# Kernel optimization log

Hardware: AMD Instinct MI355X
Metric: run time of the kernel (lower is better)

The kernel has to match this reference:

```python
import jax, jax.numpy as jnp
import numpy as np

N = 10000      # nodes
E = 100000     # edges
C = 32         # in_channels == hidden_channels == out_channels
ED = 4         # edge_dim
G = 64         # number of graphs in the batch
EPS = 1e-5     # BatchNorm eps


def setup_inputs() -> dict:
    key = jax.random.key(0)
    ks = jax.random.split(key, 20)
    rn = lambda k, shape, s=0.05: jax.random.normal(k, shape, dtype=jnp.float32) * s
    return {
        "x": jax.random.normal(ks[0], (N, C), dtype=jnp.float32),
        "edge_attr": jax.random.normal(ks[1], (E, ED), dtype=jnp.float32),
        # edge MLP 1: ED -> C -> C*C ; NNConv1 root/bias
        "e1_w1": rn(ks[2], (ED, C)), "e1_b1": jnp.zeros((C,), jnp.float32),
        "e1_w2": rn(ks[3], (C, C * C)), "e1_b2": jnp.zeros((C * C,), jnp.float32),
        "root1": rn(ks[4], (C, C)), "bias1": jnp.zeros((C,), jnp.float32),
        # edge MLP 2: ED -> C -> C*C ; NNConv2 root/bias
        "e2_w1": rn(ks[5], (ED, C)), "e2_b1": jnp.zeros((C,), jnp.float32),
        "e2_w2": rn(ks[6], (C, C * C)), "e2_b2": jnp.zeros((C * C,), jnp.float32),
        "root2": rn(ks[7], (C, C)), "bias2": jnp.zeros((C,), jnp.float32),
        # BatchNorm (eval mode: running stats)
        "bn1_g": jnp.ones((C,), jnp.float32), "bn1_b": jnp.zeros((C,), jnp.float32),
        "bn1_m": rn(ks[8], (C,), 0.1), "bn1_v": 1.0 + 0.1 * jax.random.uniform(ks[9], (C,), dtype=jnp.float32),
        "bn2_g": jnp.ones((C,), jnp.float32), "bn2_b": jnp.zeros((C,), jnp.float32),
        "bn2_m": rn(ks[10], (C,), 0.1), "bn2_v": 1.0 + 0.1 * jax.random.uniform(ks[11], (C,), dtype=jnp.float32),
        # readout: C -> C//2 -> 1
        "r1_w": rn(ks[12], (C, C // 2)), "r1_b": jnp.zeros((C // 2,), jnp.float32),
        "r2_w": rn(ks[13], (C // 2, 1)), "r2_b": jnp.zeros((1,), jnp.float32),
        "edge_index": jax.random.randint(ks[14], (2, E), 0, N),
        "batch": jnp.sort(jax.random.randint(ks[15], (N,), 0, G)),
    }


def _nnconv(x, edge_index, edge_attr, w1, b1, w2, b2, root, bias):
    # edge MLP -> per-edge weight matrix [E, C, C]
    h = jax.nn.relu(edge_attr @ w1 + b1)
    W = (h @ w2 + b2).reshape(E, C, C)
    src, dst = edge_index[0], edge_index[1]
    # gather source features, per-edge matmul, scatter-mean to target nodes
    msg = jnp.einsum('ei,eio->eo', x[src], W)                      # [E, C]
    agg = jax.ops.segment_sum(msg, dst, num_segments=N)            # [N, C]
    cnt = jax.ops.segment_sum(jnp.ones((E,), x.dtype), dst, num_segments=N)
    agg = agg / jnp.maximum(cnt, 1.0)[:, None]
    return agg + x @ root + bias


def _bn(x, g, b, m, v):
    return (x - m) * jax.lax.rsqrt(v + EPS) * g + b


def reference(x, edge_attr,
              e1_w1, e1_b1, e1_w2, e1_b2, root1, bias1,
              e2_w1, e2_b1, e2_w2, e2_b2, root2, bias2,
              bn1_g, bn1_b, bn1_m, bn1_v,
              bn2_g, bn2_b, bn2_m, bn2_v,
              r1_w, r1_b, r2_w, r2_b,
              edge_index, batch):
    h = jax.nn.relu(_bn(_nnconv(x, edge_index, edge_attr, e1_w1, e1_b1, e1_w2, e1_b2, root1, bias1),
                        bn1_g, bn1_b, bn1_m, bn1_v))
    h = jax.nn.relu(_bn(_nnconv(h, edge_index, edge_attr, e2_w1, e2_b1, e2_w2, e2_b2, root2, bias2),
                        bn2_g, bn2_b, bn2_m, bn2_v))
    # global mean pool over graphs
    psum = jax.ops.segment_sum(h, batch, num_segments=G)           # [G, C]
    pcnt = jax.ops.segment_sum(jnp.ones((N,), h.dtype), batch, num_segments=G)
    pooled = psum / jnp.maximum(pcnt, 1.0)[:, None]
    # readout MLP (dropout is identity in eval)
    return jax.nn.relu(pooled @ r1_w + r1_b) @ r2_w + r2_b          # [G, 1]
```

## Files before the change

### kernel.cpp

```cpp
#include <hip/hip_runtime.h>

#define NN 10000
#define EE 100000
#define CC 32
#define GG 64
#define EPSV 1e-5f
#define NB 8
#define SLOTS 1056
#define HST 36
#define PST 36
#define PNODE (32*PST)

__global__ void k_hist(const int* __restrict__ ei,
                       int* __restrict__ cnt, int* __restrict__ deg) {
    int t = blockIdx.x * blockDim.x + threadIdx.x;
    if (t < EE) { atomicAdd(&cnt[ei[EE + t]], 1); atomicAdd(&deg[ei[t]], 1); }
}

__global__ __launch_bounds__(1024) void k_scan(const int* __restrict__ deg,
                                               int* __restrict__ rowptr) {
    __shared__ int buf[1024];
    int t = threadIdx.x;
    int v[10]; int s = 0;
    int base = t * 10;
    #pragma unroll
    for (int k = 0; k < 10; k++) {
        int idx = base + k;
        v[k] = (idx < NN) ? deg[idx] : 0;
        s += v[k];
    }
    buf[t] = s;
    for (int off = 1; off < 1024; off <<= 1) {
        __syncthreads();
        int val = buf[t] + ((t >= off) ? buf[t - off] : 0);
        __syncthreads();
        buf[t] = val;
    }
    __syncthreads();
    int carry = (t > 0) ? buf[t - 1] : 0;
    #pragma unroll
    for (int k = 0; k < 10; k++) {
        int idx = base + k;
        if (idx < NN) rowptr[idx] = carry;
        carry += v[k];
    }
    if (t == 1023) rowptr[NN] = buf[1023];
}

__global__ void k_scatter(const int* __restrict__ ei, const int* __restrict__ rowptr,
                          int* __restrict__ cursor, int* __restrict__ csr_eid) {
    int e = blockIdx.x * blockDim.x + threadIdx.x;
    if (e >= EE) return;
    int s = ei[e];
    int pos = atomicAdd(&cursor[s], 1);
    csr_eid[rowptr[s] + pos] = e;
}

__global__ void k_w2t(const float* __restrict__ w2a, const float* __restrict__ b2a,
                      const float* __restrict__ w2b, const float* __restrict__ b2b,
                      float* __restrict__ w2r1, float* __restrict__ w2r2) {
    int s = blockIdx.x * 256 + threadIdx.x;
    int i = blockIdx.y;
    if (s >= SLOTS) return;
    float va = (s < 1024) ? w2a[(s >> 5) * 1024 + i * 32 + (s & 31)]
                          : b2a[i * 32 + (s - 1024)];
    float vb = (s < 1024) ? w2b[(s >> 5) * 1024 + i * 32 + (s & 31)]
                          : b2b[i * 32 + (s - 1024)];
    w2r1[i * SLOTS + s] = va;
    w2r2[i * SLOTS + s] = vb;
}

__global__ __launch_bounds__(256) void k_hedge2(const float* __restrict__ edge_attr,
        const float* __restrict__ w1a, const float* __restrict__ b1a,
        const float* __restrict__ w1b, const float* __restrict__ b1b,
        float* __restrict__ hbuf1, float* __restrict__ hbuf2) {
    int t = threadIdx.x;
    int e = blockIdx.x * 8 + (t >> 5);
    int o = t & 31;
    float4 a = *(const float4*)&edge_attr[(size_t)e * 4];
    float ha = fmaxf(a.x * w1a[o] + a.y * w1a[32 + o] + a.z * w1a[64 + o] + a.w * w1a[96 + o] + b1a[o], 0.f);
    float hb = fmaxf(a.x * w1b[o] + a.y * w1b[32 + o] + a.z * w1b[64 + o] + a.w * w1b[96 + o] + b1b[o], 0.f);
    hbuf1[(size_t)e * HST + o] = ha;
    hbuf2[(size_t)e * HST + o] = hb;
    if (o < 4) {
        float pad = (o == 0) ? 1.f : 0.f;
        hbuf1[(size_t)e * HST + 32 + o] = pad;
        hbuf2[(size_t)e * HST + 32 + o] = pad;
    }
}

__global__ __launch_bounds__(256, 3) void k_fused3(const float* __restrict__ x,
        const float* __restrict__ hbuf,
        const float* __restrict__ w2r,
        const int* __restrict__ ei, const int* __restrict__ rowptr,
        const int* __restrict__ csr_eid, float* __restrict__ agg) {
    __shared__ float xs[NB][32];
    __shared__ float P2[NB * PNODE];
    int t = threadIdx.x;
    int o = t & 31;
    int cb = 4 * (t >> 5);
    int n0 = blockIdx.x * NB;

    xs[t >> 5][t & 31] = x[n0 * 32 + t];
    __syncthreads();

    {
        float acc[4][NB];
        #pragma unroll
        for (int k = 0; k < 4; k++)
            #pragma unroll
            for (int n = 0; n < NB; n++) acc[k][n] = 0.f;
        #pragma unroll
        for (int j = 0; j < 8; j++) {
            float wk[4][4];
            #pragma unroll
            for (int r = 0; r < 4; r++)
                #pragma unroll
                for (int k = 0; k < 4; k++)
                    wk[r][k] = w2r[(4 * j + r) * SLOTS + (cb + k) * 32 + o];
            #pragma unroll
            for (int n = 0; n < NB; n++) {
                float4 xq = *(const float4*)&xs[n][4 * j];
                #pragma unroll
                for (int k = 0; k < 4; k++)
                    acc[k][n] += xq.x * wk[0][k] + xq.y * wk[1][k]
                               + xq.z * wk[2][k] + xq.w * wk[3][k];
            }
        }
        #pragma unroll
        for (int n = 0; n < NB; n++) {
            float4 st = make_float4(acc[0][n], acc[1][n], acc[2][n], acc[3][n]);
            *(float4*)&P2[n * PNODE + o * PST + cb] = st;
        }
    }
    if (t < 32) {
        float wb[32];
        #pragma unroll
        for (int i = 0; i < 32; i++) wb[i] = w2r[i * SLOTS + 1024 + t];
        #pragma unroll
        for (int n = 0; n < NB; n++) {
            float b = 0.f;
            #pragma unroll
            for (int j = 0; j < 8; j++) {
                float4 xq = *(const float4*)&xs[n][4 * j];
                b += xq.x * wb[4 * j] + xq.y * wb[4 * j + 1]
                   + xq.z * wb[4 * j + 2] + xq.w * wb[4 * j + 3];
            }
            *(float4*)&P2[n * PNODE + t * PST + 32] = make_float4(b, 0.f, 0.f, 0.f);
        }
    }
    __syncthreads();

    int ebase = rowptr[n0];
    int eend  = rowptr[n0 + NB];
    int grp = t >> 5;
    int pos = ebase + grp;
    int e_c = 0, src_c = 0, dst_c = 0;
    if (pos < eend) {
        e_c = csr_eid[pos];
        src_c = ei[e_c];
        dst_c = ei[EE + e_c];
    }
    while (pos < eend) {
        int pos_n = pos + 8;
        int e_n = 0, src_n = 0, dst_n = 0;
        if (pos_n < eend) {
            e_n = csr_eid[pos_n];
            src_n = ei[e_n];
            dst_n = ei[EE + e_n];
        }
        const float* Pn = &P2[(src_c - n0) * PNODE + o * PST];
        const float* hb = &hbuf[(size_t)e_c * HST];
        float4 hq[9], pq[9];
        #pragma unroll
        for (int b = 0; b < 9; b++) hq[b] = *(const float4*)&hb[4 * b];
        #pragma unroll
        for (int b = 0; b < 9; b++) pq[b] = *(const float4*)&Pn[4 * b];
        float msg = 0.f;
        #pragma unroll
        for (int b = 0; b < 9; b++)
            msg += hq[b].x * pq[b].x + hq[b].y * pq[b].y
                 + hq[b].z * pq[b].z + hq[b].w * pq[b].w;
        atomicAdd(&agg[(size_t)dst_c * 32 + o], msg);
        pos = pos_n; e_c = e_n; src_c = src_n; dst_c = dst_n;
    }
}

__global__ __launch_bounds__(256) void k_combine(const float* __restrict__ x_in,
        const float* __restrict__ agg, const int* __restrict__ cnt,
        const float* __restrict__ root, const float* __restrict__ bias,
        const float* __restrict__ bng, const float* __restrict__ bnb,
        const float* __restrict__ bnm, const float* __restrict__ bnv,
        float* __restrict__ x_out, float* __restrict__ psum,
        const int* __restrict__ batch) {
    __shared__ float xs[8][32];
    __shared__ float vals[8][32];
    __shared__ int gb[8];
    int t = threadIdx.x;
    int n0 = blockIdx.x * 8;
    xs[t >> 5][t & 31] = x_in[n0 * 32 + t];
    __syncthreads();
    int k = t >> 5, o = t & 31, n = n0 + k;
    float r = bias[o];
    #pragma unroll
    for (int i = 0; i < 32; i++) r += xs[k][i] * root[i * 32 + o];
    float a = agg[(size_t)n * 32 + o] / fmaxf((float)cnt[n], 1.f);
    float val = a + r;
    val = (val - bnm[o]) * rsqrtf(bnv[o] + EPSV) * bng[o] + bnb[o];
    val = fmaxf(val, 0.f);
    if (x_out) x_out[(size_t)n * 32 + o] = val;
    if (psum) {
        vals[k][o] = val;
        if (o == 0) gb[k] = batch[n];
        __syncthreads();
        if (k == 0) {
            float acc = vals[0][o];
            int g = gb[0];
            #pragma unroll
            for (int k2 = 1; k2 < 8; k2++) {
                if (gb[k2] == g) acc += vals[k2][o];
                else {
                    atomicAdd(&psum[(size_t)g * 32 + o], acc);
                    g = gb[k2]; acc = vals[k2][o];
                }
            }
            atomicAdd(&psum[(size_t)g * 32 + o], acc);
        }
    }
}

__global__ __launch_bounds__(256) void k_readout(const float* __restrict__ psum,
        const int* __restrict__ batch,
        const float* __restrict__ r1w, const float* __restrict__ r1b,
        const float* __restrict__ r2w, const float* __restrict__ r2b,
        float* __restrict__ out) {
    __shared__ float w1s[32 * 16];
    __shared__ float b1s[16];
    __shared__ float w2s[16];
    __shared__ float ps[GG * 32];
    int t = threadIdx.x;
    int cnt_g = 0;
    if (t < GG) {
        int lo = 0, hi = NN;
        while (lo < hi) { int m = (lo + hi) >> 1; if (batch[m] < t) lo = m + 1; else hi = m; }
        int lb = lo;
        lo = 0; hi = NN;
        while (lo < hi) { int m = (lo + hi) >> 1; if (batch[m] < t + 1) lo = m + 1; else hi = m; }
        cnt_g = lo - lb;
    }
    w1s[t] = r1w[t];
    w1s[t + 256] = r1w[t + 256];
    if (t < 16) { b1s[t] = r1b[t]; w2s[t] = r2w[t]; }
    #pragma unroll
    for (int i = 0; i < GG * 32 / 256; i++) ps[t + i * 256] = psum[t + i * 256];
    __syncthreads();
    if (t < GG) {
        float inv = 1.f / fmaxf((float)cnt_g, 1.f);
        float acc = r2b[0];
        #pragma unroll
        for (int j = 0; j < 16; j++) {
            float dot = 0.f;
            #pragma unroll
            for (int c = 0; c < 32; c++) dot += ps[t * 32 + c] * w1s[c * 16 + j];
            float z = dot * inv + b1s[j];
            acc += fmaxf(z, 0.f) * w2s[j];
        }
        out[t] = acc;
    }
}

extern "C" void kernel_launch(void* const* d_in, const int* in_sizes, int n_in,
                              void* d_out, int out_size, void* d_ws, size_t ws_size,
                              hipStream_t stream) {
    const float* x       = (const float*)d_in[0];
    const float* eattr   = (const float*)d_in[1];
    const float* e1_w1   = (const float*)d_in[2];
    const float* e1_b1   = (const float*)d_in[3];
    const float* e1_w2   = (const float*)d_in[4];
    const float* e1_b2   = (const float*)d_in[5];
    const float* root1   = (const float*)d_in[6];
    const float* bias1   = (const float*)d_in[7];
    const float* e2_w1   = (const float*)d_in[8];
    const float* e2_b1   = (const float*)d_in[9];
    const float* e2_w2   = (const float*)d_in[10];
    const float* e2_b2   = (const float*)d_in[11];
    const float* root2   = (const float*)d_in[12];
    const float* bias2   = (const float*)d_in[13];
    const float* bn1_g   = (const float*)d_in[14];
    const float* bn1_b   = (const float*)d_in[15];
    const float* bn1_m   = (const float*)d_in[16];
    const float* bn1_v   = (const float*)d_in[17];
    const float* bn2_g   = (const float*)d_in[18];
    const float* bn2_b   = (const float*)d_in[19];
    const float* bn2_m   = (const float*)d_in[20];
    const float* bn2_v   = (const float*)d_in[21];
    const float* r1_w    = (const float*)d_in[22];
    const float* r1_b    = (const float*)d_in[23];
    const float* r2_w    = (const float*)d_in[24];
    const float* r2_b    = (const float*)d_in[25];
    const int*   ei      = (const int*)d_in[26];
    const int*   batch   = (const int*)d_in[27];

    char* ws = (char*)d_ws;
    float* hbuf1  = (float*)(ws);
    float* hbuf2  = (float*)(ws + 14400000);
    float* w2r1   = (float*)(ws + 28800000);
    float* w2r2   = (float*)(ws + 28935168);
    float* agg    = (float*)(ws + 29070336);
    int*   cnt    = (int*)  (ws + 30350336);
    int*   deg    = (int*)  (ws + 30390336);
    int*   cursor = (int*)  (ws + 30430336);
    float* psum   = (float*)(ws + 30470336);
    float* xmid   = (float*)(ws + 30478528);
    int*   rowptr = (int*)  (ws + 31758528);
    int*   csr    = (int*)  (ws + 31798592);

    hipMemsetAsync(ws + 29070336, 0, 1408192, stream);

    k_hist<<<(EE + 255) / 256, 256, 0, stream>>>(ei, cnt, deg);
    k_scan<<<1, 1024, 0, stream>>>(deg, rowptr);
    k_scatter<<<(EE + 255) / 256, 256, 0, stream>>>(ei, rowptr, cursor, csr);

    dim3 wgrid((SLOTS + 255) / 256, 32);
    k_w2t<<<wgrid, 256, 0, stream>>>(e1_w2, e1_b2, e2_w2, e2_b2, w2r1, w2r2);

    k_hedge2<<<EE / 8, 256, 0, stream>>>(eattr, e1_w1, e1_b1, e2_w1, e2_b1, hbuf1, hbuf2);

    k_fused3<<<NN / NB, 256, 0, stream>>>(x, hbuf1, w2r1, ei, rowptr, csr, agg);
    k_combine<<<NN / 8, 256, 0, stream>>>(x, agg, cnt, root1, bias1,
                                          bn1_g, bn1_b, bn1_m, bn1_v,
                                          xmid, nullptr, batch);

    hipMemsetAsync(agg, 0, NN * 32 * 4, stream);
    k_fused3<<<NN / NB, 256, 0, stream>>>(xmid, hbuf2, w2r2, ei, rowptr, csr, agg);
    k_combine<<<NN / 8, 256, 0, stream>>>(xmid, agg, cnt, root2, bias2,
                                          bn2_g, bn2_b, bn2_m, bn2_v,
                                          nullptr, psum, batch);

    k_readout<<<1, 256, 0, stream>>>(psum, batch, r1_w, r1_b, r2_w, r2_b, (float*)d_out);
}
```

Baseline: 249.3 us.

## Merge setup kernels, seed CSR cursor from scan, prefetch edge features, drop agg memset

Combines the histogram, edge-MLP hidden layer and w2 transpose into a single init kernel. The scan now writes absolute cursor offsets, so the scatter no longer reads rowptr. The first combine kernel zeroes agg in place of a separate memset. The message loop software-prefetches the next edge's hidden features into registers. Together these cut launches and memsets and hide gather latency, at the cost of more register pressure in the fused kernel.

```diff
diff --git a/kernel.cpp b/kernel.cpp
--- a/kernel.cpp
+++ b/kernel.cpp
@@ -10,15 +10,55 @@
 #define HST 36
 #define PST 36
 #define PNODE (32*PST)
-
-__global__ void k_hist(const int* __restrict__ ei,
-                       int* __restrict__ cnt, int* __restrict__ deg) {
-    int t = blockIdx.x * blockDim.x + threadIdx.x;
-    if (t < EE) { atomicAdd(&cnt[ei[EE + t]], 1); atomicAdd(&deg[ei[t]], 1); }
+#define EBLK (EE/8)
+#define WBLK 160
+
+__global__ __launch_bounds__(256) void k_init(const float* __restrict__ edge_attr,
+        const float* __restrict__ w1a, const float* __restrict__ b1a,
+        const float* __restrict__ w1b, const float* __restrict__ b1b,
+        const int* __restrict__ ei,
+        float* __restrict__ hbuf1, float* __restrict__ hbuf2,
+        int* __restrict__ cnt, int* __restrict__ deg,
+        const float* __restrict__ w2a, const float* __restrict__ b2a,
+        const float* __restrict__ w2b, const float* __restrict__ b2b,
+        float* __restrict__ w2r1, float* __restrict__ w2r2) {
+    int blk = blockIdx.x;
+    int t = threadIdx.x;
+    if (blk < EBLK) {
+        int e = blk * 8 + (t >> 5);
+        int o = t & 31;
+        float4 a = *(const float4*)&edge_attr[(size_t)e * 4];
+        float ha = fmaxf(a.x * w1a[o] + a.y * w1a[32 + o] + a.z * w1a[64 + o] + a.w * w1a[96 + o] + b1a[o], 0.f);
+        float hb = fmaxf(a.x * w1b[o] + a.y * w1b[32 + o] + a.z * w1b[64 + o] + a.w * w1b[96 + o] + b1b[o], 0.f);
+        hbuf1[(size_t)e * HST + o] = ha;
+        hbuf2[(size_t)e * HST + o] = hb;
+        if (o < 4) {
+            float pad = (o == 0) ? 1.f : 0.f;
+            hbuf1[(size_t)e * HST + 32 + o] = pad;
+            hbuf2[(size_t)e * HST + 32 + o] = pad;
+        }
+        if (o == 0) {
+            atomicAdd(&cnt[ei[EE + e]], 1);
+            atomicAdd(&deg[ei[e]], 1);
+        }
+    } else {
+        int b2i = blk - EBLK;
+        int s = (b2i % 5) * 256 + t;
+        int i = b2i / 5;
+        if (s < SLOTS) {
+            float va = (s < 1024) ? w2a[(s >> 5) * 1024 + i * 32 + (s & 31)]
+                                  : b2a[i * 32 + (s - 1024)];
+            float vb = (s < 1024) ? w2b[(s >> 5) * 1024 + i * 32 + (s & 31)]
+                                  : b2b[i * 32 + (s - 1024)];
+            w2r1[i * SLOTS + s] = va;
+            w2r2[i * SLOTS + s] = vb;
+        }
+    }
 }
 
 __global__ __launch_bounds__(1024) void k_scan(const int* __restrict__ deg,
-                                               int* __restrict__ rowptr) {
+                                               int* __restrict__ rowptr,
+                                               int* __restrict__ cursor) {
     __shared__ int buf[1024];
     int t = threadIdx.x;
     int v[10]; int s = 0;
@@ -41,52 +81,18 @@
     #pragma unroll
     for (int k = 0; k < 10; k++) {
         int idx = base + k;
-        if (idx < NN) rowptr[idx] = carry;
+        if (idx < NN) { rowptr[idx] = carry; cursor[idx] = carry; }
         carry += v[k];
     }
     if (t == 1023) rowptr[NN] = buf[1023];
 }
 
-__global__ void k_scatter(const int* __restrict__ ei, const int* __restrict__ rowptr,
+__global__ void k_scatter(const int* __restrict__ ei,
                           int* __restrict__ cursor, int* __restrict__ csr_eid) {
     int e = blockIdx.x * blockDim.x + threadIdx.x;
     if (e >= EE) return;
-    int s = ei[e];
-    int pos = atomicAdd(&cursor[s], 1);
-    csr_eid[rowptr[s] + pos] = e;
-}
-
-__global__ void k_w2t(const float* __restrict__ w2a, const float* __restrict__ b2a,
-                      const float* __restrict__ w2b, const float* __restrict__ b2b,
-                      float* __restrict__ w2r1, float* __restrict__ w2r2) {
-    int s = blockIdx.x * 256 + threadIdx.x;
-    int i = blockIdx.y;
-    if (s >= SLOTS) return;
-    float va = (s < 1024) ? w2a[(s >> 5) * 1024 + i * 32 + (s & 31)]
-                          : b2a[i * 32 + (s - 1024)];
-    float vb = (s < 1024) ? w2b[(s >> 5) * 1024 + i * 32 + (s & 31)]
-                          : b2b[i * 32 + (s - 1024)];
-    w2r1[i * SLOTS + s] = va;
-    w2r2[i * SLOTS + s] = vb;
-}
-
-__global__ __launch_bounds__(256) void k_hedge2(const float* __restrict__ edge_attr,
-        const float* __restrict__ w1a, const float* __restrict__ b1a,
-        const float* __restrict__ w1b, const float* __restrict__ b1b,
-        float* __restrict__ hbuf1, float* __restrict__ hbuf2) {
-    int t = threadIdx.x;
-    int e = blockIdx.x * 8 + (t >> 5);
-    int o = t & 31;
-    float4 a = *(const float4*)&edge_attr[(size_t)e * 4];
-    float ha = fmaxf(a.x * w1a[o] + a.y * w1a[32 + o] + a.z * w1a[64 + o] + a.w * w1a[96 + o] + b1a[o], 0.f);
-    float hb = fmaxf(a.x * w1b[o] + a.y * w1b[32 + o] + a.z * w1b[64 + o] + a.w * w1b[96 + o] + b1b[o], 0.f);
-    hbuf1[(size_t)e * HST + o] = ha;
-    hbuf2[(size_t)e * HST + o] = hb;
-    if (o < 4) {
-        float pad = (o == 0) ? 1.f : 0.f;
-        hbuf1[(size_t)e * HST + 32 + o] = pad;
-        hbuf2[(size_t)e * HST + 32 + o] = pad;
-    }
+    int pos = atomicAdd(&cursor[ei[e]], 1);
+    csr_eid[pos] = e;
 }
 
 __global__ __launch_bounds__(256, 3) void k_fused3(const float* __restrict__ x,
@@ -156,38 +162,44 @@
     int grp = t >> 5;
     int pos = ebase + grp;
     int e_c = 0, src_c = 0, dst_c = 0;
+    float4 hq[9];
     if (pos < eend) {
         e_c = csr_eid[pos];
         src_c = ei[e_c];
         dst_c = ei[EE + e_c];
+        const float* hb = &hbuf[(size_t)e_c * HST];
+        #pragma unroll
+        for (int b = 0; b < 9; b++) hq[b] = *(const float4*)&hb[4 * b];
     }
     while (pos < eend) {
         int pos_n = pos + 8;
         int e_n = 0, src_n = 0, dst_n = 0;
+        float4 hq_n[9];
         if (pos_n < eend) {
             e_n = csr_eid[pos_n];
             src_n = ei[e_n];
             dst_n = ei[EE + e_n];
+            const float* hbn = &hbuf[(size_t)e_n * HST];
+            #pragma unroll
+            for (int b = 0; b < 9; b++) hq_n[b] = *(const float4*)&hbn[4 * b];
         }
         const float* Pn = &P2[(src_c - n0) * PNODE + o * PST];
-        const float* hb = &hbuf[(size_t)e_c * HST];
-        float4 hq[9], pq[9];
-        #pragma unroll
-        for (int b = 0; b < 9; b++) hq[b] = *(const float4*)&hb[4 * b];
-        #pragma unroll
-        for (int b = 0; b < 9; b++) pq[b] = *(const float4*)&Pn[4 * b];
         float msg = 0.f;
         #pragma unroll
-        for (int b = 0; b < 9; b++)
-            msg += hq[b].x * pq[b].x + hq[b].y * pq[b].y
-                 + hq[b].z * pq[b].z + hq[b].w * pq[b].w;
+        for (int b = 0; b < 9; b++) {
+            float4 pq = *(const float4*)&Pn[4 * b];
+            msg += hq[b].x * pq.x + hq[b].y * pq.y
+                 + hq[b].z * pq.z + hq[b].w * pq.w;
+        }
         atomicAdd(&agg[(size_t)dst_c * 32 + o], msg);
         pos = pos_n; e_c = e_n; src_c = src_n; dst_c = dst_n;
+        #pragma unroll
+        for (int b = 0; b < 9; b++) hq[b] = hq_n[b];
     }
 }
 
 __global__ __launch_bounds__(256) void k_combine(const float* __restrict__ x_in,
-        const float* __restrict__ agg, const int* __restrict__ cnt,
+        float* __restrict__ agg, const int* __restrict__ cnt,
         const float* __restrict__ root, const float* __restrict__ bias,
         const float* __restrict__ bng, const float* __restrict__ bnb,
         const float* __restrict__ bnm, const float* __restrict__ bnv,
@@ -208,7 +220,10 @@
     float val = a + r;
     val = (val - bnm[o]) * rsqrtf(bnv[o] + EPSV) * bng[o] + bnb[o];
     val = fmaxf(val, 0.f);
-    if (x_out) x_out[(size_t)n * 32 + o] = val;
+    if (x_out) {
+        x_out[(size_t)n * 32 + o] = val;
+        agg[(size_t)n * 32 + o] = 0.f;
+    }
     if (psum) {
         vals[k][o] = val;
         if (o == 0) gb[k] = batch[n];
@@ -309,29 +324,25 @@
     float* agg    = (float*)(ws + 29070336);
     int*   cnt    = (int*)  (ws + 30350336);
     int*   deg    = (int*)  (ws + 30390336);
-    int*   cursor = (int*)  (ws + 30430336);
-    float* psum   = (float*)(ws + 30470336);
-    float* xmid   = (float*)(ws + 30478528);
-    int*   rowptr = (int*)  (ws + 31758528);
+    float* psum   = (float*)(ws + 30430336);
+    float* xmid   = (float*)(ws + 30438528);
+    int*   rowptr = (int*)  (ws + 31718528);
+    int*   cursor = (int*)  (ws + 31758592);
     int*   csr    = (int*)  (ws + 31798592);
 
-    hipMemsetAsync(ws + 29070336, 0, 1408192, stream);
-
-    k_hist<<<(EE + 255) / 256, 256, 0, stream>>>(ei, cnt, deg);
-    k_scan<<<1, 1024, 0, stream>>>(deg, rowptr);
-    k_scatter<<<(EE + 255) / 256, 256, 0, stream>>>(ei, rowptr, cursor, csr);
-
-    dim3 wgrid((SLOTS + 255) / 256, 32);
-    k_w2t<<<wgrid, 256, 0, stream>>>(e1_w2, e1_b2, e2_w2, e2_b2, w2r1, w2r2);
-
-    k_hedge2<<<EE / 8, 256, 0, stream>>>(eattr, e1_w1, e1_b1, e2_w1, e2_b1, hbuf1, hbuf2);
+    hipMemsetAsync(ws + 29070336, 0, 1368192, stream);
+
+    k_init<<<EBLK + WBLK, 256, 0, stream>>>(eattr, e1_w1, e1_b1, e2_w1, e2_b1, ei,
+                                            hbuf1, hbuf2, cnt, deg,
+                                            e1_w2, e1_b2, e2_w2, e2_b2, w2r1, w2r2);
+    k_scan<<<1, 1024, 0, stream>>>(deg, rowptr, cursor);
+    k_scatter<<<(EE + 255) / 256, 256, 0, stream>>>(ei, cursor, csr);
 
     k_fused3<<<NN / NB, 256, 0, stream>>>(x, hbuf1, w2r1, ei, rowptr, csr, agg);
     k_combine<<<NN / 8, 256, 0, stream>>>(x, agg, cnt, root1, bias1,
                                           bn1_g, bn1_b, bn1_m, bn1_v,
                                           xmid, nullptr, batch);
 
-    hipMemsetAsync(agg, 0, NN * 32 * 4, stream);
     k_fused3<<<NN / NB, 256, 0, stream>>>(xmid, hbuf2, w2r2, ei, rowptr, csr, agg);
     k_combine<<<NN / 8, 256, 0, stream>>>(xmid, agg, cnt, root2, bias2,
                                           bn2_g, bn2_b, bn2_m, bn2_v,
```

Result: no change. 248.4 us (-0.3%).
